# Kernel tuning notes

Hardware: AMD Instinct MI355X
Metric: run time of the kernel (lower is better)

The kernel has to match this reference:

```python
import jax, jax.numpy as jnp
import numpy as np

B, S, H = 1, 4096, 2048
NH, NKV, HD = 8, 4, 256
I = 8192
EPS = 1e-6
THETA = 10000.0
WINDOW = 4096  # hardcoded sliding window for even layer_idx
LAYER_IDX = 0


def rms_norm(x, w):
    v = jnp.mean(jnp.square(x), axis=-1, keepdims=True)
    return x * jax.lax.rsqrt(v + EPS) * w


def rotate_half(x):
    h = x.shape[-1] // 2
    return jnp.concatenate([-x[..., h:], x[..., :h]], axis=-1)


def apply_rope(q, k, positions):
    # q: [B,S,NH,HD], k: [B,S,NKV,HD], positions: [B,S]
    inv_freq = 1.0 / (THETA ** (jnp.arange(0, HD, 2, dtype=jnp.float32) / HD))
    freqs = positions.astype(jnp.float32)[..., None] * inv_freq  # [B,S,HD/2]
    emb = jnp.concatenate([freqs, freqs], axis=-1)               # [B,S,HD]
    cos = jnp.cos(emb)[:, :, None, :]
    sin = jnp.sin(emb)[:, :, None, :]
    q = q * cos + rotate_half(q) * sin
    k = k * cos + rotate_half(k) * sin
    return q, k


def forward(hidden_states, q_w, k_w, v_w, o_w, gate_w, up_w, down_w, ln1_w, ln2_w,
            attention_mask, position_ids):
    # ---- input RMSNorm + attention ----
    residual = hidden_states
    x = rms_norm(hidden_states, ln1_w)

    q = (x @ q_w).reshape(B, S, NH, HD)
    k = (x @ k_w).reshape(B, S, NKV, HD)
    v = (x @ v_w).reshape(B, S, NKV, HD)
    q, k = apply_rope(q, k, position_ids)

    # GQA: repeat kv heads to match query heads
    groups = NH // NKV
    k = jnp.repeat(k, groups, axis=2)  # [B,S,NH,HD]
    v = jnp.repeat(v, groups, axis=2)

    # masks: padding mask AND causal AND (even layer) local window of WINDOW
    row = jnp.arange(S)[:, None]
    col = jnp.arange(S)[None, :]
    causal = col <= row                                   # [S,S]
    combined = causal[None, None] & (attention_mask[:, None, None, :] > 0)
    if LAYER_IDX % 2 == 0:
        keep = ~(col <= row - WINDOW)                     # mask out keys older than WINDOW
        combined = combined & keep[None, None]
    neg = jnp.finfo(jnp.float32).min
    bias = jnp.where(combined, 0.0, neg).astype(jnp.float32)  # [B,1,S,S]

    scale = HD ** -0.5
    scores = jnp.einsum('bqhd,bkhd->bhqk', q, k) * scale + bias
    probs = jax.nn.softmax(scores, axis=-1)
    attn = jnp.einsum('bhqk,bkhd->bqhd', probs, v).reshape(B, S, NH * HD)
    attn_out = attn @ o_w

    hidden_states = residual + attn_out

    # ---- post-attention RMSNorm + gated-GeLU MLP ----
    residual = hidden_states
    x = rms_norm(hidden_states, ln2_w)
    mlp = (jax.nn.gelu(x @ gate_w, approximate=True) * (x @ up_w)) @ down_w
    return residual + mlp


def setup_inputs() -> dict:
    key = jax.random.key(0)
    ks = jax.random.split(key, 9)
    std = 0.02
    n = lambda k, shp: jax.random.normal(k, shp, dtype=jnp.float32) * std
    return {
        'hidden_states': jax.random.normal(ks[0], (B, S, H), dtype=jnp.float32),
        'q_w': n(ks[1], (H, NH * HD)),
        'k_w': n(ks[2], (H, NKV * HD)),
        'v_w': n(ks[3], (H, NKV * HD)),
        'o_w': n(ks[4], (NH * HD, H)),
        'gate_w': n(ks[5], (H, I)),
        'up_w': n(ks[6], (H, I)),
        'down_w': n(ks[7], (I, H)),
        'ln1_w': jnp.ones((H,), jnp.float32),
        'ln2_w': jnp.ones((H,), jnp.float32),
        'attention_mask': jnp.ones((B, S), jnp.int32),
        'position_ids': jnp.broadcast_to(jnp.arange(S, dtype=jnp.int32)[None, :], (B, S)),
    }


def reference(hidden_states, q_w, k_w, v_w, o_w, gate_w, up_w, down_w, ln1_w, ln2_w,
              attention_mask, position_ids):
    return forward(hidden_states, q_w, k_w, v_w, o_w, gate_w, up_w, down_w,
                   ln1_w, ln2_w, attention_mask, position_ids)
```

## Files before the change

### kernel.cpp

```cpp
#include <hip/hip_runtime.h>
#include <hip/hip_bf16.h>
#include <math.h>

#define S_LEN 4096
#define HID   2048
#define NHEADS 8
#define NKVH   4
#define HDIM   256
#define FFN    8192
#define WIN    4096

typedef __bf16 bf16_t;
typedef __bf16 bf16x4 __attribute__((ext_vector_type(4)));
typedef __bf16 bf16x8 __attribute__((ext_vector_type(8)));
typedef float  floatx4 __attribute__((ext_vector_type(4)));

__device__ inline float waveReduceSum(float v) {
#pragma unroll
    for (int o = 32; o > 0; o >>= 1) v += __shfl_xor(v, o);
    return v;
}
__device__ inline float blockReduceSum(float v, float* sh) {
    int tid = threadIdx.x;
    v = waveReduceSum(v);
    if ((tid & 63) == 0) sh[tid >> 6] = v;
    __syncthreads();
    v = sh[0] + sh[1] + sh[2] + sh[3];
    __syncthreads();
    return v;
}

template <typename T>
__global__ __launch_bounds__(256) void transpose_bf16_kernel(const T* __restrict__ in,
                                                             bf16_t* __restrict__ out,
                                                             int R, int C) {
    __shared__ float tile[32][33];
    int tx = threadIdx.x & 31;
    int ty = threadIdx.x >> 5;
    int c0 = blockIdx.x * 32;
    int r0 = blockIdx.y * 32;
#pragma unroll
    for (int i = 0; i < 4; ++i)
        tile[ty + i * 8][tx] = (float)in[(long long)(r0 + ty + i * 8) * C + c0 + tx];
    __syncthreads();
#pragma unroll
    for (int i = 0; i < 4; ++i)
        out[(long long)(c0 + ty + i * 8) * R + r0 + tx] = (bf16_t)tile[tx][ty + i * 8];
}

__global__ __launch_bounds__(256) void rmsnorm_kernel(const float* __restrict__ x,
                                                      const float* __restrict__ w,
                                                      bf16_t* __restrict__ out) {
    __shared__ float sh[4];
    int row = blockIdx.x;
    const float* xr = x + (long long)row * HID;
    float v[8];
    float ss = 0.f;
#pragma unroll
    for (int i = 0; i < 8; ++i) {
        v[i] = xr[threadIdx.x + i * 256];
        ss += v[i] * v[i];
    }
    ss = blockReduceSum(ss, sh);
    float sc = rsqrtf(ss * (1.0f / HID) + 1e-6f);
#pragma unroll
    for (int i = 0; i < 8; ++i) {
        int c = threadIdx.x + i * 256;
        out[(long long)row * HID + c] = (bf16_t)(v[i] * sc * w[c]);
    }
}

__global__ __launch_bounds__(256) void rope_kernel(bf16_t* __restrict__ q,
                                                   bf16_t* __restrict__ k,
                                                   const int* __restrict__ pos_ids) {
    int s = blockIdx.x;
    float p = (float)pos_ids[s];
    for (int t = threadIdx.x; t < (NHEADS + NKVH) * (HDIM / 2); t += 256) {
        int head = t >> 7;
        int i = t & 127;
        float inv = expf(-(2.0f * (float)i / (float)HDIM) * 9.210340371976184f);
        float f = p * inv;
        float sn, cs;
        sincosf(f, &sn, &cs);
        bf16_t* base = (head < NHEADS) ? (q + (long long)s * HID + head * HDIM)
                                       : (k + (long long)s * (NKVH * HDIM) + (head - NHEADS) * HDIM);
        float a = (float)base[i];
        float b = (float)base[i + 128];
        base[i]       = (bf16_t)(a * cs - b * sn);
        base[i + 128] = (bf16_t)(b * cs + a * sn);
    }
}

__global__ __launch_bounds__(256) void flash_attn_kernel(const bf16_t* __restrict__ qg,
                                                         const bf16_t* __restrict__ kg,
                                                         const bf16_t* __restrict__ vTg,
                                                         bf16_t* __restrict__ op0,
                                                         bf16_t* __restrict__ op1,
                                                         float* __restrict__ mlb,
                                                         const int* __restrict__ amask) {
    __shared__ bf16_t sK[64 * 256];
    __shared__ bf16_t sV[256 * 64];
    __shared__ bf16_t sPb[4 * 16 * 72];

    const int h = blockIdx.y;
    const int kh = blockIdx.z;
    const int tid = threadIdx.x;
    const int lane = tid & 63;
    const int w = tid >> 6;
    const int tl = lane & 15;
    const int quad = lane >> 4;

    const bf16_t* Qh = qg + h * HDIM;
    const bf16_t* Kh = kg + (h >> 1) * HDIM;
    const bf16_t* Vh = vTg + (long long)(h >> 1) * HDIM * S_LEN;
    bf16_t* Op = kh ? op1 : op0;
    bf16_t* sP = sPb + w * (16 * 72);

#pragma unroll 1
    for (int half = 0; half < 2; ++half) {
        const int qi = half ? (63 - blockIdx.x) : blockIdx.x;
        const int qr0 = qi * 64;
        const int ntiles = qi + 1;
        const int mid = ntiles >> 1;
        const int t0 = kh ? mid : 0;
        const int t1 = kh ? ntiles : mid;
        const int irow = qr0 + w * 16 + tl;

        const bf16_t* qrow = Qh + (long long)irow * HID;
        bf16x8 qf[8];
#pragma unroll
        for (int ks = 0; ks < 8; ++ks)
            qf[ks] = *(const bf16x8*)(qrow + (ks * 4 + quad) * 8);

        floatx4 oacc[16] = {};
        float m_i = -3e38f, l_i = 0.f;

        bf16x8 stK[8], stV[8];
        auto load_tile = [&](int kt) {
#pragma unroll
            for (int it = 0; it < 8; ++it) {
                int s = it * 256 + tid;
                {
                    int m = s >> 5, sg = s & 31, g = sg ^ (m & 7);
                    stK[it] = *(const bf16x8*)(Kh + (long long)(kt + m) * (NKVH * HDIM) + g * 8);
                }
                {
                    int m = s >> 3, sg = s & 7, g = sg ^ (m & 7);
                    stV[it] = *(const bf16x8*)(Vh + (long long)m * S_LEN + kt + g * 8);
                }
            }
        };

        if (t0 < t1) load_tile(t0 * 64);

#pragma unroll 1
        for (int t = t0; t < t1; ++t) {
            const int kt = t * 64;
#pragma unroll
            for (int it = 0; it < 8; ++it) {
                int s = it * 256 + tid;
                *(bf16x8*)(sK + s * 8) = stK[it];
                *(bf16x8*)(sV + s * 8) = stV[it];
            }
            __syncthreads();

            if (t + 1 < t1) load_tile((t + 1) * 64);
            __builtin_amdgcn_sched_barrier(0);

            floatx4 sacc[4] = {};
            __builtin_amdgcn_s_setprio(1);
#pragma unroll
            for (int ks = 0; ks < 8; ++ks) {
                bf16x8 kf[4];
#pragma unroll
                for (int ni = 0; ni < 4; ++ni) {
                    int row = ni * 16 + tl;
                    int ph = (ks * 4 + quad) ^ (row & 7);
                    kf[ni] = *(const bf16x8*)(sK + row * 256 + ph * 8);
                }
#pragma unroll
                for (int ni = 0; ni < 4; ++ni)
                    sacc[ni] = __builtin_amdgcn_mfma_f32_16x16x32_bf16(kf[ni], qf[ks], sacc[ni], 0, 0, 0);
            }
            __builtin_amdgcn_s_setprio(0);

            float sv[4][4];
            float mx = -3e38f;
#pragma unroll
            for (int ni = 0; ni < 4; ++ni) {
                int4 am = *(const int4*)(amask + kt + ni * 16 + quad * 4);
#pragma unroll
                for (int r = 0; r < 4; ++r) {
                    int j = kt + ni * 16 + quad * 4 + r;
                    int amr = (r == 0) ? am.x : (r == 1) ? am.y : (r == 2) ? am.z : am.w;
                    bool valid = (j <= irow) && (j > irow - WIN) && (amr > 0);
                    float x = valid ? sacc[ni][r] * 0.0625f : -3e38f;
                    sv[ni][r] = x;
                    mx = fmaxf(mx, x);
                }
            }
            mx = fmaxf(mx, __shfl_xor(mx, 16));
            mx = fmaxf(mx, __shfl_xor(mx, 32));
            bool noresc = __all(mx <= m_i + 8.0f);
            float mnew = noresc ? m_i : fmaxf(m_i, mx);
            float rs = 0.f;
#pragma unroll
            for (int ni = 0; ni < 4; ++ni) {
                bf16x4 pk;
#pragma unroll
                for (int r = 0; r < 4; ++r) {
                    float p = (sv[ni][r] > -1e37f) ? __expf(sv[ni][r] - mnew) : 0.f;
                    rs += p;
                    pk[r] = (bf16_t)p;
                }
                *(bf16x4*)(sP + tl * 72 + ni * 16 + quad * 4) = pk;
            }
            rs += __shfl_xor(rs, 16);
            rs += __shfl_xor(rs, 32);
            if (noresc) {
                l_i += rs;
            } else {
                float alpha = __expf(m_i - mnew);
                l_i = l_i * alpha + rs;
                m_i = mnew;
                floatx4 av;
#pragma unroll
                for (int r = 0; r < 4; ++r) av[r] = __shfl(alpha, quad * 4 + r);
#pragma unroll
                for (int dt = 0; dt < 16; ++dt) oacc[dt] *= av;
            }

            __builtin_amdgcn_s_setprio(1);
#pragma unroll
            for (int k2 = 0; k2 < 2; ++k2) {
                bf16x8 pf = *(const bf16x8*)(sP + tl * 72 + k2 * 32 + quad * 8);
#pragma unroll
                for (int dt = 0; dt < 16; ++dt) {
                    int d = dt * 16 + tl;
                    int ph = (k2 * 4 + quad) ^ (d & 7);
                    bf16x8 vf = *(const bf16x8*)(sV + d * 64 + ph * 8);
                    oacc[dt] = __builtin_amdgcn_mfma_f32_16x16x32_bf16(pf, vf, oacc[dt], 0, 0, 0);
                }
            }
            __builtin_amdgcn_s_setprio(0);
            __syncthreads();
        }

        floatx4 inv;
#pragma unroll
        for (int r = 0; r < 4; ++r) {
            float lv = __shfl(l_i, quad * 4 + r);
            inv[r] = (lv > 0.f) ? 1.0f / lv : 0.f;
        }
#pragma unroll
        for (int dt = 0; dt < 16; ++dt) {
#pragma unroll
            for (int r = 0; r < 4; ++r) {
                long long row = qr0 + w * 16 + quad * 4 + r;
                Op[row * HID + h * HDIM + dt * 16 + tl] = (bf16_t)(oacc[dt][r] * inv[r]);
            }
        }
        if (quad == 0) {
            long long mi = ((long long)(kh * NHEADS + h) * S_LEN + qr0 + w * 16 + tl) * 2;
            mlb[mi] = m_i;
            mlb[mi + 1] = l_i;
        }
    }
}

__global__ __launch_bounds__(256) void combine_kernel(bf16_t* __restrict__ op0,
                                                      const bf16_t* __restrict__ op1,
                                                      const float* __restrict__ mlb) {
    int h = blockIdx.x;
    int row = blockIdx.y;
    int d = threadIdx.x;
    long long m0i = ((long long)h * S_LEN + row) * 2;
    long long m1i = ((long long)(NHEADS + h) * S_LEN + row) * 2;
    float m0 = mlb[m0i], l0 = mlb[m0i + 1];
    float m1 = mlb[m1i], l1 = mlb[m1i + 1];
    float M = fmaxf(m0, m1);
    float w0 = (l0 > 0.f) ? l0 * __expf(m0 - M) : 0.f;
    float w1 = (l1 > 0.f) ? l1 * __expf(m1 - M) : 0.f;
    float inv = 1.0f / (w0 + w1);
    long long idx = (long long)row * HID + h * HDIM + d;
    float v = (w0 * (float)op0[idx] + w1 * (float)op1[idx]) * inv;
    op0[idx] = (bf16_t)v;
}

template <int MODE>
__global__ __launch_bounds__(256) void gemm_kernel(const bf16_t* __restrict__ A, int lda,
                                                   const bf16_t* __restrict__ Bt, int ldb,
                                                   void* __restrict__ Cv, int ldc,
                                                   const void* __restrict__ aux, int K) {
    __shared__ bf16_t smem[2 * 128 * 64];
    bf16_t* sA = smem;
    bf16_t* sB = smem + 128 * 64;

    const int tid = threadIdx.x;
    const int n0 = blockIdx.x * 128;
    const int m0 = blockIdx.y * 128;

    const int lane = tid & 63;
    const int wid = tid >> 6;
    const int wm = (wid >> 1) * 64;
    const int wn = (wid & 1) * 64;
    const int tl = lane & 15;
    const int quad = lane >> 4;

    floatx4 acc[4][4] = {};

    for (int k0 = 0; k0 < K; k0 += 64) {
#pragma unroll
        for (int it = 0; it < 4; ++it) {
            int s = it * 256 + tid;
            int m = s >> 3;
            int sg = s & 7;
            int g = sg ^ (m & 7);
            const bf16_t* ga = A + (long long)(m0 + m) * lda + k0 + g * 8;
            __builtin_amdgcn_global_load_lds((const __attribute__((address_space(1))) void*)ga,
                                             (__attribute__((address_space(3))) void*)(sA + s * 8),
                                             16, 0, 0);
            const bf16_t* gb = Bt + (long long)(n0 + m) * ldb + k0 + g * 8;
            __builtin_amdgcn_global_load_lds((const __attribute__((address_space(1))) void*)gb,
                                             (__attribute__((address_space(3))) void*)(sB + s * 8),
                                             16, 0, 0);
        }
        __builtin_amdgcn_s_waitcnt(0x0f70);
        __syncthreads();

#pragma unroll
        for (int kk = 0; kk < 2; ++kk) {
            bf16x8 af[4], bfr[4];
#pragma unroll
            for (int mi = 0; mi < 4; ++mi) {
                int m = wm + mi * 16 + tl;
                int sg = (kk * 4 + quad) ^ (m & 7);
                af[mi] = *(const bf16x8*)(sA + m * 64 + sg * 8);
            }
#pragma unroll
            for (int ni = 0; ni < 4; ++ni) {
                int n = wn + ni * 16 + tl;
                int sg = (kk * 4 + quad) ^ (n & 7);
                bfr[ni] = *(const bf16x8*)(sB + n * 64 + sg * 8);
            }
#pragma unroll
            for (int mi = 0; mi < 4; ++mi)
#pragma unroll
                for (int ni = 0; ni < 4; ++ni)
                    acc[mi][ni] = __builtin_amdgcn_mfma_f32_16x16x32_bf16(af[mi], bfr[ni], acc[mi][ni], 0, 0, 0);
        }
        __syncthreads();
    }

#pragma unroll
    for (int mi = 0; mi < 4; ++mi) {
#pragma unroll
        for (int ni = 0; ni < 4; ++ni) {
#pragma unroll
            for (int r = 0; r < 4; ++r) {
                int gr = m0 + wm + mi * 16 + quad * 4 + r;
                int gc = n0 + wn + ni * 16 + tl;
                long long idx = (long long)gr * ldc + gc;
                float v = acc[mi][ni][r];
                if (MODE == 0) {
                    ((bf16_t*)Cv)[idx] = (bf16_t)v;
                } else if (MODE == 1) {
                    ((float*)Cv)[idx] = ((const float*)aux)[idx] + v;
                } else {
                    float g = (float)((const bf16_t*)aux)[idx];
                    float t = 0.7978845608028654f * (g + 0.044715f * g * g * g);
                    float ge = 0.5f * g * (1.0f + tanhf(t));
                    ((bf16_t*)Cv)[idx] = (bf16_t)(ge * v);
                }
            }
        }
    }
}

extern "C" void kernel_launch(void* const* d_in, const int* in_sizes, int n_in,
                              void* d_out, int out_size, void* d_ws, size_t ws_size,
                              hipStream_t stream) {
    const float* hidden = (const float*)d_in[0];
    const float* q_w    = (const float*)d_in[1];
    const float* k_w    = (const float*)d_in[2];
    const float* v_w    = (const float*)d_in[3];
    const float* o_w    = (const float*)d_in[4];
    const float* gate_w = (const float*)d_in[5];
    const float* up_w   = (const float*)d_in[6];
    const float* down_w = (const float*)d_in[7];
    const float* ln1_w  = (const float*)d_in[8];
    const float* ln2_w  = (const float*)d_in[9];
    const int* amask    = (const int*)d_in[10];
    const int* pos_ids  = (const int*)d_in[11];
    float* out = (float*)d_out;

    const size_t MB = 1ull << 20;
    char* ws = (char*)d_ws;
    bf16_t* wqT = (bf16_t*)(ws + 0 * MB);
    bf16_t* wkT = (bf16_t*)(ws + 8 * MB);
    bf16_t* wvT = (bf16_t*)(ws + 12 * MB);
    bf16_t* woT = (bf16_t*)(ws + 16 * MB);
    bf16_t* wgT = (bf16_t*)(ws + 24 * MB);
    bf16_t* wuT = (bf16_t*)(ws + 56 * MB);
    bf16_t* wdT = (bf16_t*)(ws + 88 * MB);
    bf16_t* xb    = (bf16_t*)(ws + 120 * MB);
    bf16_t* qb    = (bf16_t*)(ws + 136 * MB);
    bf16_t* kb    = (bf16_t*)(ws + 152 * MB);
    bf16_t* vb    = (bf16_t*)(ws + 160 * MB);
    bf16_t* vT    = (bf16_t*)(ws + 168 * MB);
    bf16_t* op0   = (bf16_t*)(ws + 120 * MB);
    bf16_t* op1   = (bf16_t*)(ws + 176 * MB);
    float*  mlb   = (float*) (ws + 192 * MB);
    bf16_t* attnb = (bf16_t*)(ws + 120 * MB);
    bf16_t* xb2   = (bf16_t*)(ws + 120 * MB);
    bf16_t* gateb = (bf16_t*)(ws + 136 * MB);
    (void)ws_size; (void)in_sizes; (void)n_in; (void)out_size;

    dim3 blk(256);

    transpose_bf16_kernel<float><<<dim3(64, 64), blk, 0, stream>>>(q_w, wqT, 2048, 2048);
    transpose_bf16_kernel<float><<<dim3(32, 64), blk, 0, stream>>>(k_w, wkT, 2048, 1024);
    transpose_bf16_kernel<float><<<dim3(32, 64), blk, 0, stream>>>(v_w, wvT, 2048, 1024);
    transpose_bf16_kernel<float><<<dim3(64, 64), blk, 0, stream>>>(o_w, woT, 2048, 2048);
    transpose_bf16_kernel<float><<<dim3(256, 64), blk, 0, stream>>>(gate_w, wgT, 2048, 8192);
    transpose_bf16_kernel<float><<<dim3(256, 64), blk, 0, stream>>>(up_w, wuT, 2048, 8192);
    transpose_bf16_kernel<float><<<dim3(64, 256), blk, 0, stream>>>(down_w, wdT, 8192, 2048);

    rmsnorm_kernel<<<dim3(S_LEN), blk, 0, stream>>>(hidden, ln1_w, xb);

    gemm_kernel<0><<<dim3(16, 32), blk, 0, stream>>>(xb, HID, wqT, HID, qb, 2048, nullptr, HID);
    gemm_kernel<0><<<dim3(8, 32), blk, 0, stream>>>(xb, HID, wkT, HID, kb, 1024, nullptr, HID);
    gemm_kernel<0><<<dim3(8, 32), blk, 0, stream>>>(xb, HID, wvT, HID, vb, 1024, nullptr, HID);

    rope_kernel<<<dim3(S_LEN), blk, 0, stream>>>(qb, kb, pos_ids);

    transpose_bf16_kernel<bf16_t><<<dim3(32, 128), blk, 0, stream>>>(vb, vT, S_LEN, 1024);

    flash_attn_kernel<<<dim3(32, NHEADS, 2), blk, 0, stream>>>(qb, kb, vT, op0, op1, mlb, amask);
    combine_kernel<<<dim3(NHEADS, S_LEN), blk, 0, stream>>>(op0, op1, mlb);

    gemm_kernel<1><<<dim3(16, 32), blk, 0, stream>>>(attnb, 2048, woT, 2048, out, 2048, hidden, 2048);

    rmsnorm_kernel<<<dim3(S_LEN), blk, 0, stream>>>(out, ln2_w, xb2);

    gemm_kernel<0><<<dim3(64, 32), blk, 0, stream>>>(xb2, HID, wgT, HID, gateb, FFN, nullptr, HID);
    gemm_kernel<2><<<dim3(64, 32), blk, 0, stream>>>(xb2, HID, wuT, HID, gateb, FFN, gateb, HID);
    gemm_kernel<1><<<dim3(16, 32), blk, 0, stream>>>(gateb, FFN, wdT, FFN, out, 2048, out, FFN);
}
```

Baseline: 1.306 ms.

## Fuse QKV projections into one GEMM and double-buffer GEMM shared memory

Merges the separate Q, K and V projection GEMMs into a single GEMM writing a packed [S,4096] QKV buffer. This relies on the transposed wq, wk and wv weights sitting contiguously in the workspace, and rope, the V transpose and attention now read through the combined stride. Separately, the GEMM kernel gains two shared-memory stages so the async global-to-LDS load of the next K tile overlaps the MFMA work on the current one, with explicit waitcnt and barriers. The intent is fewer launches, better GPU fill for the small K and V GEMMs, and hidden load latency. The cost is twice the LDS per block, which may lower occupancy.

New measurement: 1.152 ms. -11.8%, faster.

```diff
diff --git a/kernel.cpp b/kernel.cpp
--- a/kernel.cpp
+++ b/kernel.cpp
@@ -9,11 +9,16 @@
 #define HDIM   256
 #define FFN    8192
 #define WIN    4096
+#define QKV_LD 4096
 
 typedef __bf16 bf16_t;
 typedef __bf16 bf16x4 __attribute__((ext_vector_type(4)));
 typedef __bf16 bf16x8 __attribute__((ext_vector_type(8)));
 typedef float  floatx4 __attribute__((ext_vector_type(4)));
+
+#define WAITCNT_VM0   0x0f70
+#define WAITCNT_VM8   0x0f78
+#define WAITCNT_LGKM0 0xc07f
 
 __device__ inline float waveReduceSum(float v) {
 #pragma unroll
@@ -33,7 +38,7 @@
 template <typename T>
 __global__ __launch_bounds__(256) void transpose_bf16_kernel(const T* __restrict__ in,
                                                              bf16_t* __restrict__ out,
-                                                             int R, int C) {
+                                                             int ldin, int ldout) {
     __shared__ float tile[32][33];
     int tx = threadIdx.x & 31;
     int ty = threadIdx.x >> 5;
@@ -41,11 +46,11 @@
     int r0 = blockIdx.y * 32;
 #pragma unroll
     for (int i = 0; i < 4; ++i)
-        tile[ty + i * 8][tx] = (float)in[(long long)(r0 + ty + i * 8) * C + c0 + tx];
+        tile[ty + i * 8][tx] = (float)in[(long long)(r0 + ty + i * 8) * ldin + c0 + tx];
     __syncthreads();
 #pragma unroll
     for (int i = 0; i < 4; ++i)
-        out[(long long)(c0 + ty + i * 8) * R + r0 + tx] = (bf16_t)tile[tx][ty + i * 8];
+        out[(long long)(c0 + ty + i * 8) * ldout + r0 + tx] = (bf16_t)tile[tx][ty + i * 8];
 }
 
 __global__ __launch_bounds__(256) void rmsnorm_kernel(const float* __restrict__ x,
@@ -70,8 +75,7 @@
     }
 }
 
-__global__ __launch_bounds__(256) void rope_kernel(bf16_t* __restrict__ q,
-                                                   bf16_t* __restrict__ k,
+__global__ __launch_bounds__(256) void rope_kernel(bf16_t* __restrict__ qkv,
                                                    const int* __restrict__ pos_ids) {
     int s = blockIdx.x;
     float p = (float)pos_ids[s];
@@ -82,8 +86,8 @@
         float f = p * inv;
         float sn, cs;
         sincosf(f, &sn, &cs);
-        bf16_t* base = (head < NHEADS) ? (q + (long long)s * HID + head * HDIM)
-                                       : (k + (long long)s * (NKVH * HDIM) + (head - NHEADS) * HDIM);
+        int col = (head < NHEADS) ? head * HDIM : HID + (head - NHEADS) * HDIM;
+        bf16_t* base = qkv + (long long)s * QKV_LD + col;
         float a = (float)base[i];
         float b = (float)base[i + 128];
         base[i]       = (bf16_t)(a * cs - b * sn);
@@ -91,8 +95,7 @@
     }
 }
 
-__global__ __launch_bounds__(256) void flash_attn_kernel(const bf16_t* __restrict__ qg,
-                                                         const bf16_t* __restrict__ kg,
+__global__ __launch_bounds__(256) void flash_attn_kernel(const bf16_t* __restrict__ qkv,
                                                          const bf16_t* __restrict__ vTg,
                                                          bf16_t* __restrict__ op0,
                                                          bf16_t* __restrict__ op1,
@@ -110,8 +113,8 @@
     const int tl = lane & 15;
     const int quad = lane >> 4;
 
-    const bf16_t* Qh = qg + h * HDIM;
-    const bf16_t* Kh = kg + (h >> 1) * HDIM;
+    const bf16_t* Qh = qkv + h * HDIM;
+    const bf16_t* Kh = qkv + HID + (h >> 1) * HDIM;
     const bf16_t* Vh = vTg + (long long)(h >> 1) * HDIM * S_LEN;
     bf16_t* Op = kh ? op1 : op0;
     bf16_t* sP = sPb + w * (16 * 72);
@@ -126,7 +129,7 @@
         const int t1 = kh ? ntiles : mid;
         const int irow = qr0 + w * 16 + tl;
 
-        const bf16_t* qrow = Qh + (long long)irow * HID;
+        const bf16_t* qrow = Qh + (long long)irow * QKV_LD;
         bf16x8 qf[8];
 #pragma unroll
         for (int ks = 0; ks < 8; ++ks)
@@ -142,7 +145,7 @@
                 int s = it * 256 + tid;
                 {
                     int m = s >> 5, sg = s & 31, g = sg ^ (m & 7);
-                    stK[it] = *(const bf16x8*)(Kh + (long long)(kt + m) * (NKVH * HDIM) + g * 8);
+                    stK[it] = *(const bf16x8*)(Kh + (long long)(kt + m) * QKV_LD + g * 8);
                 }
                 {
                     int m = s >> 3, sg = s & 7, g = sg ^ (m & 7);
@@ -292,9 +295,7 @@
                                                    const bf16_t* __restrict__ Bt, int ldb,
                                                    void* __restrict__ Cv, int ldc,
                                                    const void* __restrict__ aux, int K) {
-    __shared__ bf16_t smem[2 * 128 * 64];
-    bf16_t* sA = smem;
-    bf16_t* sB = smem + 128 * 64;
+    __shared__ bf16_t smem[2][2 * 128 * 64];
 
     const int tid = threadIdx.x;
     const int n0 = blockIdx.x * 128;
@@ -309,7 +310,9 @@
 
     floatx4 acc[4][4] = {};
 
-    for (int k0 = 0; k0 < K; k0 += 64) {
+    auto stage = [&](int buf, int k0) {
+        bf16_t* sA = smem[buf];
+        bf16_t* sB = smem[buf] + 128 * 64;
 #pragma unroll
         for (int it = 0; it < 4; ++it) {
             int s = it * 256 + tid;
@@ -325,9 +328,23 @@
                                              (__attribute__((address_space(3))) void*)(sB + s * 8),
                                              16, 0, 0);
         }
-        __builtin_amdgcn_s_waitcnt(0x0f70);
-        __syncthreads();
-
+    };
+
+    stage(0, 0);
+    int cur = 0;
+
+    for (int k0 = 0; k0 < K; k0 += 64) {
+        if (k0 + 64 < K) {
+            stage(cur ^ 1, k0 + 64);
+            __builtin_amdgcn_s_waitcnt(WAITCNT_VM8);
+        } else {
+            __builtin_amdgcn_s_waitcnt(WAITCNT_VM0);
+        }
+        __builtin_amdgcn_s_barrier();
+        __builtin_amdgcn_sched_barrier(0);
+
+        const bf16_t* sA = smem[cur];
+        const bf16_t* sB = smem[cur] + 128 * 64;
 #pragma unroll
         for (int kk = 0; kk < 2; ++kk) {
             bf16x8 af[4], bfr[4];
@@ -349,7 +366,11 @@
                 for (int ni = 0; ni < 4; ++ni)
                     acc[mi][ni] = __builtin_amdgcn_mfma_f32_16x16x32_bf16(af[mi], bfr[ni], acc[mi][ni], 0, 0, 0);
         }
-        __syncthreads();
+
+        __builtin_amdgcn_s_waitcnt(WAITCNT_LGKM0);
+        __builtin_amdgcn_sched_barrier(0);
+        __builtin_amdgcn_s_barrier();
+        cur ^= 1;
     }
 
 #pragma unroll
@@ -404,9 +425,7 @@
     bf16_t* wuT = (bf16_t*)(ws + 56 * MB);
     bf16_t* wdT = (bf16_t*)(ws + 88 * MB);
     bf16_t* xb    = (bf16_t*)(ws + 120 * MB);
-    bf16_t* qb    = (bf16_t*)(ws + 136 * MB);
-    bf16_t* kb    = (bf16_t*)(ws + 152 * MB);
-    bf16_t* vb    = (bf16_t*)(ws + 160 * MB);
+    bf16_t* qkvb  = (bf16_t*)(ws + 136 * MB);
     bf16_t* vT    = (bf16_t*)(ws + 168 * MB);
     bf16_t* op0   = (bf16_t*)(ws + 120 * MB);
     bf16_t* op1   = (bf16_t*)(ws + 176 * MB);
@@ -419,24 +438,22 @@
     dim3 blk(256);
 
     transpose_bf16_kernel<float><<<dim3(64, 64), blk, 0, stream>>>(q_w, wqT, 2048, 2048);
-    transpose_bf16_kernel<float><<<dim3(32, 64), blk, 0, stream>>>(k_w, wkT, 2048, 1024);
-    transpose_bf16_kernel<float><<<dim3(32, 64), blk, 0, stream>>>(v_w, wvT, 2048, 1024);
+    transpose_bf16_kernel<float><<<dim3(32, 64), blk, 0, stream>>>(k_w, wkT, 1024, 2048);
+    transpose_bf16_kernel<float><<<dim3(32, 64), blk, 0, stream>>>(v_w, wvT, 1024, 2048);
     transpose_bf16_kernel<float><<<dim3(64, 64), blk, 0, stream>>>(o_w, woT, 2048, 2048);
-    transpose_bf16_kernel<float><<<dim3(256, 64), blk, 0, stream>>>(gate_w, wgT, 2048, 8192);
-    transpose_bf16_kernel<float><<<dim3(256, 64), blk, 0, stream>>>(up_w, wuT, 2048, 8192);
-    transpose_bf16_kernel<float><<<dim3(64, 256), blk, 0, stream>>>(down_w, wdT, 8192, 2048);
+    transpose_bf16_kernel<float><<<dim3(256, 64), blk, 0, stream>>>(gate_w, wgT, 8192, 2048);
+    transpose_bf16_kernel<float><<<dim3(256, 64), blk, 0, stream>>>(up_w, wuT, 8192, 2048);
+    transpose_bf16_kernel<float><<<dim3(64, 256), blk, 0, stream>>>(down_w, wdT, 2048, 8192);
 
     rmsnorm_kernel<<<dim3(S_LEN), blk, 0, stream>>>(hidden, ln1_w, xb);
 
-    gemm_kernel<0><<<dim3(16, 32), blk, 0, stream>>>(xb, HID, wqT, HID, qb, 2048, nullptr, HID);
-    gemm_kernel<0><<<dim3(8, 32), blk, 0, stream>>>(xb, HID, wkT, HID, kb, 1024, nullptr, HID);
-    gemm_kernel<0><<<dim3(8, 32), blk, 0, stream>>>(xb, HID, wvT, HID, vb, 1024, nullptr, HID);
-
-    rope_kernel<<<dim3(S_LEN), blk, 0, stream>>>(qb, kb, pos_ids);
-
-    transpose_bf16_kernel<bf16_t><<<dim3(32, 128), blk, 0, stream>>>(vb, vT, S_LEN, 1024);
-
-    flash_attn_kernel<<<dim3(32, NHEADS, 2), blk, 0, stream>>>(qb, kb, vT, op0, op1, mlb, amask);
+    gemm_kernel<0><<<dim3(32, 32), blk, 0, stream>>>(xb, HID, wqT, HID, qkvb, QKV_LD, nullptr, HID);
+
+    rope_kernel<<<dim3(S_LEN), blk, 0, stream>>>(qkvb, pos_ids);
+
+    transpose_bf16_kernel<bf16_t><<<dim3(32, 128), blk, 0, stream>>>(qkvb + 3072, vT, QKV_LD, S_LEN);
+
+    flash_attn_kernel<<<dim3(32, NHEADS, 2), blk, 0, stream>>>(qkvb, vT, op0, op1, mlb, amask);
     combine_kernel<<<dim3(NHEADS, S_LEN), blk, 0, stream>>>(op0, op1, mlb);
 
     gemm_kernel<1><<<dim3(16, 32), blk, 0, stream>>>(attnb, 2048, woT, 2048, out, 2048, hidden, 2048);
```
